# Kernel tuning notes

Hardware: AMD Instinct MI355X
Metric: run time of the kernel (lower is better)

The kernel has to match this reference:

```python
import jax, jax.numpy as jnp
import numpy as np

# Production-scale dims: N tokens = 64 batch x 8192 seq, hidden width 256.
N, D_IN, D_OUT = 524288, 256, 256
P_NONZERO = 0.05  # mimics bnn.random.calc_desired_var -> sparse ternary W


def binarise(v):
    # bnn.functions.binarise forward: sign with binarise(0) = +1
    return jnp.where(v >= 0, 1.0, -1.0).astype(v.dtype)


def setup_inputs() -> dict:
    key = jax.random.key(0)
    kx, kw = jax.random.split(key)
    # x: binary activations in {-1,+1} (output of a previous binarise layer)
    x = jnp.where(jax.random.normal(kx, (N, D_IN)) >= 0, 1.0, -1.0).astype(jnp.float32)
    # W: ternary {-1, 0, +1} with Var = P_NONZERO (values +-1 each w.p. p/2)
    u = jax.random.uniform(kw, (D_IN, D_OUT))
    W = jnp.where(u < P_NONZERO / 2, -1.0,
                  jnp.where(u < P_NONZERO, 1.0, 0.0)).astype(jnp.float32)
    return {"x": x, "W": W}


def reference(x, W):
    # integer = x @ W  (ternary-weight matmul; int math in torch, same values in fp32)
    integer = x @ W  # [N, D_OUT]
    return binarise(integer)
```

## Files before the change

### kernel.cpp

```cpp
#include <hip/hip_runtime.h>
#include <stdint.h>


#define NROWS 524288
#define DDIM  256

typedef uint32_t u32;
typedef unsigned long long u64;

__global__ __launch_bounds__(256, 3)
void ternbin_kernel(const float* __restrict__ x, const float* __restrict__ W,
                    float* __restrict__ out) {
    __shared__ u32 ldsA[DDIM][9];
    __shared__ u32 ldsM[DDIM][9];
    __shared__ int ldsC[DDIM];

    const int t = threadIdx.x;

    {
        u32 A[8] = {0,0,0,0,0,0,0,0};
        u32 M[8] = {0,0,0,0,0,0,0,0};
        #pragma unroll 8
        for (int k = 0; k < DDIM; ++k) {
            const float v = W[k * DDIM + t];
            const int   w = ((k & 3) << 1) | (k >> 7);
            const u32 bit = 1u << ((k >> 2) & 31);
            if (v != 0.0f) A[w] |= bit;
            if (v <  0.0f) M[w] |= bit;
        }
        int c = 0;
        #pragma unroll
        for (int w = 0; w < 8; ++w) {
            ldsA[t][w] = A[w];
            ldsM[t][w] = M[w];
            c += __popc(A[w]);
        }
        ldsC[t] = c;
    }
    __syncthreads();

    const int lane = t & 63;
    u32 A[4][8], M[4][8];
    int C[4];
    #pragma unroll
    for (int jc = 0; jc < 4; ++jc) {
        const int col = 4 * lane + jc;
        #pragma unroll
        for (int w = 0; w < 8; ++w) {
            A[jc][w] = ldsA[col][w];
            M[jc][w] = ldsM[col][w];
        }
        C[jc] = ldsC[col];
    }
    __syncthreads();

    const int gwave = (int)((blockIdx.x * blockDim.x + (unsigned)t) >> 6);
    const float* xp = x   + (size_t)gwave * 64 * DDIM + 4 * lane;
    float*       op = out + (size_t)gwave * 64 * DDIM + 4 * lane;

    #pragma unroll 1
    for (int it = 0; it < 16; ++it) {
        uint4 xv[4];
        #pragma unroll
        for (int rr = 0; rr < 4; ++rr)
            xv[rr] = *reinterpret_cast<const uint4*>(xp + (size_t)(4 * it + rr) * DDIM);

        #pragma unroll
        for (int rr = 0; rr < 4; ++rr) {
            const u64 b0 = __ballot((int)xv[rr].x < 0);
            const u64 b1 = __ballot((int)xv[rr].y < 0);
            const u64 b2 = __ballot((int)xv[rr].z < 0);
            const u64 b3 = __ballot((int)xv[rr].w < 0);
            u32 s[8];
            s[0] = (u32)b0; s[1] = (u32)(b0 >> 32);
            s[2] = (u32)b1; s[3] = (u32)(b1 >> 32);
            s[4] = (u32)b2; s[5] = (u32)(b2 >> 32);
            s[6] = (u32)b3; s[7] = (u32)(b3 >> 32);

            u32 o[4];
            #pragma unroll
            for (int jc = 0; jc < 4; ++jc) {
                int p = 0;
                #pragma unroll
                for (int w = 0; w < 8; ++w)
                    p += __popc((s[w] ^ M[jc][w]) & A[jc][w]);
                const int d = C[jc] - 2 * p;
                o[jc] = 0x3f800000u | ((u32)d & 0x80000000u);
            }
            uint4 ov;
            ov.x = o[0]; ov.y = o[1]; ov.z = o[2]; ov.w = o[3];
            *reinterpret_cast<uint4*>(op + (size_t)(4 * it + rr) * DDIM) = ov;
        }
    }
}

extern "C" void kernel_launch(void* const* d_in, const int* in_sizes, int n_in,
                              void* d_out, int out_size, void* d_ws, size_t ws_size,
                              hipStream_t stream) {
    const float* x = (const float*)d_in[0];
    const float* W = (const float*)d_in[1];
    float* out = (float*)d_out;
    ternbin_kernel<<<2048, 256, 0, stream>>>(x, W, out);
}
```

Before: 1.087 ms.

## Give each wave a column slice and share row loads across block waves

Measured after the change: 936.6 us. 1.16x faster.

```diff
diff --git a/kernel.cpp b/kernel.cpp
--- a/kernel.cpp
+++ b/kernel.cpp
@@ -4,66 +4,46 @@
 
 #define NROWS 524288
 #define DDIM  256
+#define BLOCKS 2048
+#define ROWS_PER_BLOCK (NROWS / BLOCKS)
+#define ITERS (ROWS_PER_BLOCK / 4)
 
 typedef uint32_t u32;
 typedef unsigned long long u64;
 
-__global__ __launch_bounds__(256, 3)
+__global__ __launch_bounds__(256, 4)
 void ternbin_kernel(const float* __restrict__ x, const float* __restrict__ W,
                     float* __restrict__ out) {
-    __shared__ u32 ldsA[DDIM][9];
-    __shared__ u32 ldsM[DDIM][9];
-    __shared__ int ldsC[DDIM];
+    const int t    = threadIdx.x;
+    const int lane = t & 63;
+    const int wv   = t >> 6;
+    const int col  = (wv << 6) | lane;
 
-    const int t = threadIdx.x;
+    u32 A[8] = {0,0,0,0,0,0,0,0};
+    u32 M[8] = {0,0,0,0,0,0,0,0};
+    #pragma unroll 8
+    for (int k = 0; k < DDIM; ++k) {
+        const float v = W[k * DDIM + col];
+        const int   w = ((k & 3) << 1) | (k >> 7);
+        const u32 bit = 1u << ((k >> 2) & 31);
+        if (v != 0.0f) A[w] |= bit;
+        if (v <  0.0f) M[w] |= bit;
+    }
+    int C = 0;
+    #pragma unroll
+    for (int w = 0; w < 8; ++w) C += __popc(A[w]);
 
-    {
-        u32 A[8] = {0,0,0,0,0,0,0,0};
-        u32 M[8] = {0,0,0,0,0,0,0,0};
-        #pragma unroll 8
-        for (int k = 0; k < DDIM; ++k) {
-            const float v = W[k * DDIM + t];
-            const int   w = ((k & 3) << 1) | (k >> 7);
-            const u32 bit = 1u << ((k >> 2) & 31);
-            if (v != 0.0f) A[w] |= bit;
-            if (v <  0.0f) M[w] |= bit;
-        }
-        int c = 0;
-        #pragma unroll
-        for (int w = 0; w < 8; ++w) {
-            ldsA[t][w] = A[w];
-            ldsM[t][w] = M[w];
-            c += __popc(A[w]);
-        }
-        ldsC[t] = c;
-    }
-    __syncthreads();
-
-    const int lane = t & 63;
-    u32 A[4][8], M[4][8];
-    int C[4];
-    #pragma unroll
-    for (int jc = 0; jc < 4; ++jc) {
-        const int col = 4 * lane + jc;
-        #pragma unroll
-        for (int w = 0; w < 8; ++w) {
-            A[jc][w] = ldsA[col][w];
-            M[jc][w] = ldsM[col][w];
-        }
-        C[jc] = ldsC[col];
-    }
-    __syncthreads();
-
-    const int gwave = (int)((blockIdx.x * blockDim.x + (unsigned)t) >> 6);
-    const float* xp = x   + (size_t)gwave * 64 * DDIM + 4 * lane;
-    float*       op = out + (size_t)gwave * 64 * DDIM + 4 * lane;
+    const size_t row0 = (size_t)blockIdx.x * ROWS_PER_BLOCK;
+    const float* xp = x   + row0 * DDIM + 4 * lane;
+    float*       op = out + row0 * DDIM + col;
 
     #pragma unroll 1
-    for (int it = 0; it < 16; ++it) {
+    for (int it = 0; it < ITERS; ++it) {
+        const int rbase = it << 2;
         uint4 xv[4];
         #pragma unroll
         for (int rr = 0; rr < 4; ++rr)
-            xv[rr] = *reinterpret_cast<const uint4*>(xp + (size_t)(4 * it + rr) * DDIM);
+            xv[rr] = *reinterpret_cast<const uint4*>(xp + (size_t)(rbase + rr) * DDIM);
 
         #pragma unroll
         for (int rr = 0; rr < 4; ++rr) {
@@ -71,25 +51,24 @@
             const u64 b1 = __ballot((int)xv[rr].y < 0);
             const u64 b2 = __ballot((int)xv[rr].z < 0);
             const u64 b3 = __ballot((int)xv[rr].w < 0);
-            u32 s[8];
-            s[0] = (u32)b0; s[1] = (u32)(b0 >> 32);
-            s[2] = (u32)b1; s[3] = (u32)(b1 >> 32);
-            s[4] = (u32)b2; s[5] = (u32)(b2 >> 32);
-            s[6] = (u32)b3; s[7] = (u32)(b3 >> 32);
+            const u32 s0 = (u32)b0, s1 = (u32)(b0 >> 32);
+            const u32 s2 = (u32)b1, s3 = (u32)(b1 >> 32);
+            const u32 s4 = (u32)b2, s5 = (u32)(b2 >> 32);
+            const u32 s6 = (u32)b3, s7 = (u32)(b3 >> 32);
 
-            u32 o[4];
-            #pragma unroll
-            for (int jc = 0; jc < 4; ++jc) {
-                int p = 0;
-                #pragma unroll
-                for (int w = 0; w < 8; ++w)
-                    p += __popc((s[w] ^ M[jc][w]) & A[jc][w]);
-                const int d = C[jc] - 2 * p;
-                o[jc] = 0x3f800000u | ((u32)d & 0x80000000u);
-            }
-            uint4 ov;
-            ov.x = o[0]; ov.y = o[1]; ov.z = o[2]; ov.w = o[3];
-            *reinterpret_cast<uint4*>(op + (size_t)(4 * it + rr) * DDIM) = ov;
+            int p = 0;
+            p += __popc((s0 ^ M[0]) & A[0]);
+            p += __popc((s1 ^ M[1]) & A[1]);
+            p += __popc((s2 ^ M[2]) & A[2]);
+            p += __popc((s3 ^ M[3]) & A[3]);
+            p += __popc((s4 ^ M[4]) & A[4]);
+            p += __popc((s5 ^ M[5]) & A[5]);
+            p += __popc((s6 ^ M[6]) & A[6]);
+            p += __popc((s7 ^ M[7]) & A[7]);
+            const int d = C - 2 * p;
+            const u32 o = 0x3f800000u | ((u32)d & 0x80000000u);
+            __builtin_nontemporal_store(o,
+                reinterpret_cast<u32*>(op + (size_t)(rbase + rr) * DDIM));
         }
     }
 }
@@ -100,5 +79,5 @@
     const float* x = (const float*)d_in[0];
     const float* W = (const float*)d_in[1];
     float* out = (float*)d_out;
-    ternbin_kernel<<<2048, 256, 0, stream>>>(x, W, out);
+    ternbin_kernel<<<BLOCKS, 256, 0, stream>>>(x, W, out);
 }
```
